# Optimization experiments

Measured on AMD Instinct MI355X. Metric: run time of the kernel, lower is better.

The kernel has to match this reference:

```python
import jax, jax.numpy as jnp
import numpy as np

B, N_KV, N_Q = 32, 4096, 8
D_INP, D_SLOT, HEADS, MLP_H = 256, 256, 4, 1024
ITERS = 3
EPS = 1e-8


def _ln(x, g, b, eps=1e-5):
    m = jnp.mean(x, axis=-1, keepdims=True)
    v = jnp.var(x, axis=-1, keepdims=True)
    return (x - m) * jax.lax.rsqrt(v + eps) * g + b


def setup_inputs() -> dict:
    key = jax.random.key(0)
    ks = jax.random.split(key, 12)
    def w(k, shape, fan_in):
        return jax.random.normal(k, shape, jnp.float32) / np.float32(np.sqrt(fan_in))
    return {
        "inputs": jax.random.normal(ks[0], (B, N_KV, D_INP), jnp.float32),
        "slots": jax.random.normal(ks[1], (B, N_Q, D_SLOT), jnp.float32),
        "ln_in_g": jnp.ones((D_INP,), jnp.float32), "ln_in_b": jnp.zeros((D_INP,), jnp.float32),
        "ln_slot_g": jnp.ones((D_SLOT,), jnp.float32), "ln_slot_b": jnp.zeros((D_SLOT,), jnp.float32),
        "ln_mlp_g": jnp.ones((D_SLOT,), jnp.float32), "ln_mlp_b": jnp.zeros((D_SLOT,), jnp.float32),
        "Wq": w(ks[2], (D_SLOT, D_SLOT), D_SLOT),
        "Wk": w(ks[3], (D_SLOT, D_INP), D_INP),
        "Wv": w(ks[4], (D_SLOT, D_INP), D_INP),
        "W_ih": w(ks[5], (3 * D_SLOT, D_SLOT), D_SLOT),
        "W_hh": w(ks[6], (3 * D_SLOT, D_SLOT), D_SLOT),
        "b_ih": jnp.zeros((3 * D_SLOT,), jnp.float32),
        "b_hh": jnp.zeros((3 * D_SLOT,), jnp.float32),
        "W1": w(ks[7], (MLP_H, D_SLOT), D_SLOT), "b1": jnp.zeros((MLP_H,), jnp.float32),
        "W2": w(ks[8], (D_SLOT, MLP_H), MLP_H), "b2": jnp.zeros((D_SLOT,), jnp.float32),
    }


def reference(inputs, slots, ln_in_g, ln_in_b, ln_slot_g, ln_slot_b, ln_mlp_g, ln_mlp_b,
              Wq, Wk, Wv, W_ih, W_hh, b_ih, b_hh, W1, b1, W2, b2):
    Bb, Nkv, _ = inputs.shape
    _, Nq, Ds = slots.shape
    hd = Ds // HEADS

    x = _ln(inputs, ln_in_g, ln_in_b)
    # k, v: [B, H, N_kv, hd]; k pre-scaled by hd**-0.5 as in the original
    k = (x @ Wk.T).reshape(Bb, Nkv, HEADS, hd).transpose(0, 2, 1, 3) * (hd ** -0.5)
    v = (x @ Wv.T).reshape(Bb, Nkv, HEADS, hd).transpose(0, 2, 1, 3)

    attn_vis = attn_temp = None
    for it in range(ITERS):
        if it == ITERS - 1:
            slots = jax.lax.stop_gradient(slots)
        slots_prev = slots
        s = _ln(slots, ln_slot_g, ln_slot_b)
        q = (s @ Wq.T).reshape(Bb, Nq, HEADS, hd).transpose(0, 2, 1, 3)  # [B,H,Nq,hd]
        logits = jnp.einsum('bhnd,bhqd->bhnq', k, q)  # [B,H,Nkv,Nq]
        # competing softmax: normalize jointly over (head, slot) per input token
        lt = logits.transpose(0, 2, 1, 3).reshape(Bb, Nkv, HEADS * Nq)
        attn = jax.nn.softmax(lt, axis=-1).reshape(Bb, Nkv, HEADS, Nq).transpose(0, 2, 1, 3)
        attn_vis = attn.sum(axis=1)   # [B, Nkv, Nq]
        attn_temp = attn_vis          # original recomputes the identical softmax; same values
        a = attn + EPS
        a = a / a.sum(axis=-2, keepdims=True)  # renormalize over N_kv
        updates = jnp.einsum('bhnq,bhnd->bhqd', a, v).transpose(0, 2, 1, 3).reshape(Bb, Nq, Ds)
        # GRU cell (torch GRUCell math)
        gx = updates @ W_ih.T + b_ih
        gh = slots_prev @ W_hh.T + b_hh
        xr, xz, xn = jnp.split(gx, 3, axis=-1)
        hr, hz, hn = jnp.split(gh, 3, axis=-1)
        r = jax.nn.sigmoid(xr + hr)
        z = jax.nn.sigmoid(xz + hz)
        n = jnp.tanh(xn + r * hn)
        slots = (1.0 - z) * n + z * slots_prev
        # MLP with residual
        m = _ln(slots, ln_mlp_g, ln_mlp_b)
        slots = slots + (jax.nn.relu(m @ W1.T + b1) @ W2.T + b2)
    return slots, attn_vis, attn_temp
```

## Files before the change

### kernel.cpp

```cpp
#include <hip/hip_runtime.h>
#include <math.h>


#define NKV   4096
#define DD    256
#define HQN   32
#define EPSR  1e-8f

#define WS_V      0
#define WS_A0     262144
#define WS_A1     263168
#define WS_C0     264192
#define WS_C1     265216
#define WS_SLOTA  266240
#define WS_SLOTB  331776
#define WS_WQT    397312
#define WS_QF     462848
#define WS_WPGXH  528384
#define WS_WFT    921600
#define WS_WHHT   1314816
#define WS_W1T    1413120
#define WS_W2T    1544192
#define WS_RS     1675264
#define WS_RM     1806336

typedef float f32x4 __attribute__((ext_vector_type(4)));
typedef short s16x8 __attribute__((ext_vector_type(8)));
typedef int   v2i   __attribute__((ext_vector_type(2)));

__device__ __forceinline__ unsigned bfr(float f) {
    unsigned u = __float_as_uint(f);
    return (u + 0x7fffu + ((u >> 16) & 1u)) >> 16;
}
__device__ __forceinline__ unsigned pk2(float lo, float hi) {
    return bfr(lo) | (bfr(hi) << 16);
}
__device__ __forceinline__ float bf2f(unsigned short us) {
    return __uint_as_float((unsigned)us << 16);
}
__device__ __forceinline__ float bflo(unsigned u) { return __uint_as_float(u << 16); }
__device__ __forceinline__ float bfhi(unsigned u) { return __uint_as_float(u & 0xffff0000u); }

__device__ __forceinline__ v2i tr_read(unsigned addr) {
    v2i d;
    asm volatile("ds_read_b64_tr_b16 %0, %1" : "=v"(d) : "v"(addr));
    return d;
}
__device__ __forceinline__ s16x8 mk_frag(v2i a, v2i b) {
    union { int i[4]; s16x8 s; } u;
    u.i[0] = a.x; u.i[1] = a.y; u.i[2] = b.x; u.i[3] = b.y;
    return u.s;
}

__global__ __launch_bounds__(256) void k_copy(const float* __restrict__ in,
                                              float* __restrict__ out, int n) {
    int i = blockIdx.x * 256 + threadIdx.x;
    if (i < n) out[i] = in[i];
}

__global__ __launch_bounds__(256) void k_tr(const float* __restrict__ in,
                                            float* __restrict__ out, int R, int C) {
    __shared__ float tile[32][33];
    int bx = blockIdx.x * 32, by = blockIdx.y * 32;
    int x = bx + threadIdx.x;
    for (int k = 0; k < 32; k += 8) {
        int y = by + threadIdx.y + k;
        if (x < C && y < R) tile[threadIdx.y + k][threadIdx.x] = in[(size_t)y * C + x];
    }
    __syncthreads();
    int r = by + threadIdx.x;
    for (int k = 0; k < 32; k += 8) {
        int c = bx + threadIdx.y + k;
        if (c < C && r < R) out[(size_t)c * R + r] = tile[threadIdx.x][threadIdx.y + k];
    }
}

__global__ __launch_bounds__(256) void k_wfold(
    const float* __restrict__ Wih, const float* __restrict__ Wv,
    unsigned* __restrict__ WfT2)
{
    __shared__ float wr[256];
    const int c = blockIdx.x, t = threadIdx.x;
    wr[t] = Wih[(size_t)c * 256 + t];
    __syncthreads();
    const float2* wv2 = (const float2*)Wv;
    #pragma unroll
    for (int pp = 0; pp < 2; ++pp) {
        int P = pp * 256 + t;
        int h = P >> 7, p = P & 127;
        float f0 = 0.f, f1 = 0.f;
        #pragma unroll 8
        for (int d = 0; d < 64; ++d) {
            float a = wr[h * 64 + d];
            float2 v = wv2[(size_t)(h * 64 + d) * 128 + p];
            f0 = fmaf(a, v.x, f0); f1 = fmaf(a, v.y, f1);
        }
        WfT2[(size_t)P * 768 + c] = pk2(f0, f1);
    }
}

__global__ __launch_bounds__(256) void k_trpack(
    const float* __restrict__ in, unsigned* __restrict__ out, int R, int C)
{
    const int c2 = blockIdx.x;
    const int t = threadIdx.x;
    for (int q = 0; q < R / 256; ++q) {
        int r = q * 256 + t;
        out[(size_t)c2 * R + r] = pk2(in[(size_t)r * C + 2 * c2],
                                      in[(size_t)r * C + 2 * c2 + 1]);
    }
}

__global__ __launch_bounds__(256) void k_prep_a(
    const float* __restrict__ slots, const float* __restrict__ g_s, const float* __restrict__ b_s,
    const float* __restrict__ wqt, float* __restrict__ qf_g,
    float* __restrict__ V_g, float* __restrict__ A0_g, float* __restrict__ A1_g)
{
    __shared__ float s_row[256];
    __shared__ float red[8];
    const int t = threadIdx.x;
    const int b = blockIdx.x, qi = blockIdx.y;
    const int lane = t & 63, w = t >> 6;

    #pragma unroll
    for (int h = 0; h < 4; ++h)
        V_g[((size_t)b * 32 + h * 8 + qi) * 256 + t] = 0.f;
    if (t < 4) { A0_g[b * 32 + t * 8 + qi] = 0.f; A1_g[b * 32 + t * 8 + qi] = 0.f; }

    float v = slots[((size_t)b * 8 + qi) * 256 + t];
    float s0 = v, s1 = v * v;
    #pragma unroll
    for (int o = 32; o >= 1; o >>= 1) { s0 += __shfl_xor(s0, o, 64); s1 += __shfl_xor(s1, o, 64); }
    if (lane == 0) { red[w] = s0; red[4 + w] = s1; }
    __syncthreads();
    {
        float m = (red[0] + red[1] + red[2] + red[3]) * (1.f / 256.f);
        float q2 = (red[4] + red[5] + red[6] + red[7]) * (1.f / 256.f);
        float rs = rsqrtf(q2 - m * m + 1e-5f);
        s_row[t] = (v - m) * rs * g_s[t] + b_s[t];
    }
    __syncthreads();

    float a = 0.f;
    #pragma unroll 8
    for (int j = 0; j < 256; ++j)
        a = fmaf(s_row[j], wqt[j * 256 + t], a);
    qf_g[((size_t)b * 8 + qi) * 256 + t] = a;
}

__global__ __launch_bounds__(256) void k_prep_b(
    const float* __restrict__ qf_g, const float* __restrict__ Wk,
    const float* __restrict__ g_in, const float* __restrict__ b_in,
    unsigned short* __restrict__ wp_bf, float* __restrict__ c0_g, float* __restrict__ c1_g)
{
    __shared__ float qs[512];
    __shared__ float redc[4096];
    const int t = threadIdx.x;
    const int b = blockIdx.x, h = blockIdx.y;
    const int lane = t & 63, w = t >> 6;
    const float LNS = 0.125f * 1.44269504f;

    #pragma unroll
    for (int rep = 0; rep < 2; ++rep) {
        int idx = rep * 256 + t;
        int qi = idx >> 6, d = idx & 63;
        qs[idx] = qf_g[((size_t)b * 8 + qi) * 256 + h * 64 + d];
    }
    __syncthreads();

    float a2[8];
    #pragma unroll
    for (int qi = 0; qi < 8; ++qi) a2[qi] = 0.f;
    #pragma unroll 4
    for (int d = 0; d < 64; ++d) {
        float wv = Wk[(size_t)(h * 64 + d) * 256 + t];
        #pragma unroll
        for (int qi = 0; qi < 8; ++qi) a2[qi] = fmaf(qs[qi * 64 + d], wv, a2[qi]);
    }
    const float gv = g_in[t], bv = b_in[t];
    #pragma unroll
    for (int qi = 0; qi < 8; ++qi) {
        float kv = LNS * a2[qi];
        float we = kv * gv;
        wp_bf[((size_t)b * HQN + h * 8 + qi) * 256 + t] = (unsigned short)bfr(we);
        redc[qi * 256 + t] = we;
        redc[2048 + qi * 256 + t] = kv * bv;
    }
    __syncthreads();
    #pragma unroll
    for (int rep = 0; rep < 2; ++rep) {
        int r = w * 2 + rep;
        float sv1 = redc[r * 256 + lane] + redc[r * 256 + 64 + lane] +
                    redc[r * 256 + 128 + lane] + redc[r * 256 + 192 + lane];
        float sv0 = redc[2048 + r * 256 + lane] + redc[2048 + r * 256 + 64 + lane] +
                    redc[2048 + r * 256 + 128 + lane] + redc[2048 + r * 256 + 192 + lane];
        #pragma unroll
        for (int o = 32; o >= 1; o >>= 1) {
            sv1 += __shfl_xor(sv1, o, 64);
            sv0 += __shfl_xor(sv0, o, 64);
        }
        if (lane == 0) {
            c1_g[b * 32 + h * 8 + r] = sv1;
            c0_g[b * 32 + h * 8 + r] = sv0;
        }
    }
}

template<int STATS, int WVIS>
__global__ __launch_bounds__(256, 4) void k_attn(
    const float* __restrict__ inp, const unsigned short* __restrict__ wp_bf,
    const float* __restrict__ c0_g, const float* __restrict__ c1_g,
    float* __restrict__ V_g, float* __restrict__ A0_g, float* __restrict__ A1_g,
    float* __restrict__ rs_g, float* __restrict__ rm_g,
    float* __restrict__ out_vis, float* __restrict__ out_temp)
{
    __shared__ unsigned short xb[16 * 520];
    __shared__ unsigned short wl[8192];
    __shared__ unsigned short pt[1024];
    __shared__ float stats[64];
    __shared__ float redm[64];
    __shared__ float reds[64];

    const int t = threadIdx.x;
    const int l = t & 63, w = t >> 6;
    const int g = l >> 4, li = l & 15;
    const int b = blockIdx.y, kb = blockIdx.x;

    char* xbB = (char*)xb;
    char* wlB = (char*)wl;
    char* ptB = (char*)pt;
    const int tok_s = t >> 3, seg8 = t & 7;

    {
        const uint4* wp4 = (const uint4*)wp_bf + ((size_t)b * 8192 + (t >> 3) * 256 + (t & 7) * 32) / 8;
        const int hq = t >> 3, sg = t & 7;
        #pragma unroll
        for (int q = 0; q < 4; ++q) {
            uint4 v = wp4[q];
            *(uint4*)(wlB + hq * 512 + (((sg * 4 + q) ^ (hq & 7)) * 16)) = v;
        }
    }

    const int Mt = w & 1, Nt = w >> 1;
    const int hqB = Nt * 16 + li;
    const float c0r = c0_g[b * 32 + hqB];
    const float c1r = c1_g[b * 32 + hqB];
    const int MtV = w >> 1, ntb = (w & 1) * 8;
    const int hqA = MtV * 16 + li;

    f32x4 av[8];
    #pragma unroll
    for (int u = 0; u < 8; ++u) av[u] = (f32x4){0.f, 0.f, 0.f, 0.f};
    float A0acc = 0.f, A1acc = 0.f;

    const unsigned xbase = (unsigned)(uintptr_t)xbB;
    const int cbase = kb * 4;

    #pragma unroll
    for (int ci = 0; ci < 4; ++ci) {
        const int n0 = (cbase + ci) * 32;

        const float4* row4 = (const float4*)(inp + ((size_t)b * NKV + n0 + tok_s) * 256);
        float4 ld[8];
        #pragma unroll
        for (int u = 0; u < 8; ++u) ld[u] = row4[(u >> 2) * 32 + seg8 * 4 + (u & 3)];

        if (!STATS) {
            if (t < 32) stats[t] = rs_g[b * 4096 + n0 + t];
            else if (t < 64) stats[t] = rm_g[b * 4096 + n0 + t - 32];
        }
        #pragma unroll
        for (int c = 0; c < 2; ++c) {
            int nt = seg8 + 8 * c;
            #pragma unroll
            for (int h = 0; h < 2; ++h) {
                float4 fa = ld[c * 4 + h * 2], fb = ld[c * 4 + h * 2 + 1];
                uint4 pk;
                pk.x = pk2(fa.x, fa.y); pk.y = pk2(fa.z, fa.w);
                pk.z = pk2(fb.x, fb.y); pk.w = pk2(fb.z, fb.w);
                *(uint4*)(xbB + nt * 1040 + tok_s * 32 + h * 16) = pk;
            }
        }
        if (STATS) {
            float s0 = 0.f, s1 = 0.f;
            #pragma unroll
            for (int u = 0; u < 8; ++u) {
                float4 v = ld[u];
                s0 += v.x + v.y + v.z + v.w;
                s1 = fmaf(v.x, v.x, s1); s1 = fmaf(v.y, v.y, s1);
                s1 = fmaf(v.z, v.z, s1); s1 = fmaf(v.w, v.w, s1);
            }
            s0 += __shfl_xor(s0, 1, 64); s1 += __shfl_xor(s1, 1, 64);
            s0 += __shfl_xor(s0, 2, 64); s1 += __shfl_xor(s1, 2, 64);
            s0 += __shfl_xor(s0, 4, 64); s1 += __shfl_xor(s1, 4, 64);
            float m  = s0 * (1.f / 256.f);
            float rs = rsqrtf(s1 * (1.f / 256.f) - m * m + 1e-5f);
            if (seg8 == 0) {
                stats[tok_s] = rs;
                stats[32 + tok_s] = rs * m;
                rs_g[b * 4096 + n0 + tok_s] = rs;
                rm_g[b * 4096 + n0 + tok_s] = rs * m;
            }
        }
        __syncthreads();

        f32x4 accS = (f32x4){0.f, 0.f, 0.f, 0.f};
        #pragma unroll
        for (int kk = 0; kk < 8; ++kk) {
            s16x8 af = *(const s16x8*)(xbB + (kk * 2 + (g >> 1)) * 1040 +
                                       (Mt * 16 + li) * 32 + (g & 1) * 16);
            s16x8 bf = *(const s16x8*)(wlB + hqB * 512 + (((kk * 4 + g) ^ (hqB & 7)) * 16));
            accS = __builtin_amdgcn_mfma_f32_16x16x32_bf16(af, bf, accS, 0, 0, 0);
        }

        float lg[4], rsv[4], rmv[4], mh[4], ex[4], aa[4];
        #pragma unroll
        for (int r = 0; r < 4; ++r) {
            int tokr = Mt * 16 + g * 4 + r;
            rsv[r] = stats[tokr];
            rmv[r] = stats[32 + tokr];
            lg[r] = fmaf(rsv[r], accS[r], fmaf(-rmv[r], c1r, c0r));
        }
        #pragma unroll
        for (int r = 0; r < 4; ++r) {
            float v = lg[r];
            v = fmaxf(v, __shfl_xor(v, 1, 64));
            v = fmaxf(v, __shfl_xor(v, 2, 64));
            v = fmaxf(v, __shfl_xor(v, 4, 64));
            v = fmaxf(v, __shfl_xor(v, 8, 64));
            mh[r] = v;
            ex[r] = exp2f(lg[r] - v);
            float s = ex[r];
            s += __shfl_xor(s, 1, 64);
            s += __shfl_xor(s, 2, 64);
            s += __shfl_xor(s, 4, 64);
            s += __shfl_xor(s, 8, 64);
            if (li == 0) {
                int tokr = Mt * 16 + g * 4 + r;
                redm[tokr * 2 + Nt] = v;
                reds[tokr * 2 + Nt] = s;
            }
        }
        __syncthreads();
        #pragma unroll
        for (int r = 0; r < 4; ++r) {
            int tokr = Mt * 16 + g * 4 + r;
            float m0 = redm[tokr * 2], m1 = redm[tokr * 2 + 1];
            float mx = fmaxf(m0, m1);
            float tot = reds[tokr * 2] * exp2f(m0 - mx) + reds[tokr * 2 + 1] * exp2f(m1 - mx);
            aa[r] = ex[r] * (exp2f(mh[r] - mx) / tot);
            A0acc += aa[r];
            A1acc = fmaf(aa[r], rmv[r], A1acc);
        }
        {
            uint2 pw;
            pw.x = pk2(aa[0] * rsv[0], aa[1] * rsv[1]);
            pw.y = pk2(aa[2] * rsv[2], aa[3] * rsv[3]);
            int tokb = Mt * 16 + g * 4;
            int slot = (tokb >> 3) ^ ((hqB >> 1) & 3);
            *(uint2*)(ptB + hqB * 64 + slot * 16 + (tokb & 7) * 2) = pw;
        }
        __syncthreads();

        if (WVIS) {
            int tk = t >> 3, q = t & 7;
            float sv = 0.f;
            #pragma unroll
            for (int h = 0; h < 4; ++h) {
                int hq = h * 8 + q;
                int slot = (tk >> 3) ^ ((hq >> 1) & 3);
                sv += bf2f(*(const unsigned short*)(ptB + hq * 64 + slot * 16 + (tk & 7) * 2));
            }
            float vv = sv / stats[tk];
            size_t o = ((size_t)b * NKV + n0 + tk) * 8 + q;
            out_vis[o] = vv; out_temp[o] = vv;
        }

        {
            s16x8 pa = *(const s16x8*)(ptB + hqA * 64 + ((g ^ ((hqA >> 1) & 3)) * 16));
            unsigned abase = xbase + g * 256 + li * 8;
            v2i t0a = tr_read(abase + (ntb + 0) * 1040);
            v2i t0b = tr_read(abase + (ntb + 0) * 1040 + 128);
            v2i t1a = tr_read(abase + (ntb + 1) * 1040);
            v2i t1b = tr_read(abase + (ntb + 1) * 1040 + 128);
            v2i t2a = tr_read(abase + (ntb + 2) * 1040);
            v2i t2b = tr_read(abase + (ntb + 2) * 1040 + 128);
            v2i t3a = tr_read(abase + (ntb + 3) * 1040);
            v2i t3b = tr_read(abase + (ntb + 3) * 1040 + 128);
            asm volatile("s_waitcnt lgkmcnt(0)" ::: "memory");
            __builtin_amdgcn_sched_barrier(0);
            av[0] = __builtin_amdgcn_mfma_f32_16x16x32_bf16(pa, mk_frag(t0a, t0b), av[0], 0, 0, 0);
            av[1] = __builtin_amdgcn_mfma_f32_16x16x32_bf16(pa, mk_frag(t1a, t1b), av[1], 0, 0, 0);
            av[2] = __builtin_amdgcn_mfma_f32_16x16x32_bf16(pa, mk_frag(t2a, t2b), av[2], 0, 0, 0);
            av[3] = __builtin_amdgcn_mfma_f32_16x16x32_bf16(pa, mk_frag(t3a, t3b), av[3], 0, 0, 0);
            v2i t4a = tr_read(abase + (ntb + 4) * 1040);
            v2i t4b = tr_read(abase + (ntb + 4) * 1040 + 128);
            v2i t5a = tr_read(abase + (ntb + 5) * 1040);
            v2i t5b = tr_read(abase + (ntb + 5) * 1040 + 128);
            v2i t6a = tr_read(abase + (ntb + 6) * 1040);
            v2i t6b = tr_read(abase + (ntb + 6) * 1040 + 128);
            v2i t7a = tr_read(abase + (ntb + 7) * 1040);
            v2i t7b = tr_read(abase + (ntb + 7) * 1040 + 128);
            asm volatile("s_waitcnt lgkmcnt(0)" ::: "memory");
            __builtin_amdgcn_sched_barrier(0);
            av[4] = __builtin_amdgcn_mfma_f32_16x16x32_bf16(pa, mk_frag(t4a, t4b), av[4], 0, 0, 0);
            av[5] = __builtin_amdgcn_mfma_f32_16x16x32_bf16(pa, mk_frag(t5a, t5b), av[5], 0, 0, 0);
            av[6] = __builtin_amdgcn_mfma_f32_16x16x32_bf16(pa, mk_frag(t6a, t6b), av[6], 0, 0, 0);
            av[7] = __builtin_amdgcn_mfma_f32_16x16x32_bf16(pa, mk_frag(t7a, t7b), av[7], 0, 0, 0);
        }
        __syncthreads();
    }

    A0acc += __shfl_xor(A0acc, 16, 64); A0acc += __shfl_xor(A0acc, 32, 64);
    A1acc += __shfl_xor(A1acc, 16, 64); A1acc += __shfl_xor(A1acc, 32, 64);
    if (g == 0) {
        atomicAdd(A0_g + b * 32 + hqB, A0acc);
        atomicAdd(A1_g + b * 32 + hqB, A1acc);
    }
    #pragma unroll
    for (int i = 0; i < 8; ++i) {
        int j = (ntb + i) * 16 + li;
        #pragma unroll
        for (int r = 0; r < 4; ++r) {
            int hq = MtV * 16 + g * 4 + r;
            atomicAdd(V_g + ((size_t)b * 32 + hq) * 256 + j, av[i][r]);
        }
    }
}

__global__ __launch_bounds__(256) void k_gates(
    const float* __restrict__ V_g, const float* __restrict__ A0_g,
    const float* __restrict__ A1_g,
    const float* __restrict__ g_in, const float* __restrict__ b_in,
    const float* __restrict__ slot_cur,
    const unsigned* __restrict__ WfT2, const unsigned* __restrict__ WhhT2,
    float* __restrict__ gxh, float* __restrict__ slot_nxt)
{
    __shared__ __align__(16) float aT[1024 * 4];
    const int t = threadIdx.x;
    const int rg = blockIdx.y;
    const int chunk = blockIdx.x;
    const int row0 = rg * 4;
    float acc0 = 0.f, acc1 = 0.f, acc2 = 0.f, acc3 = 0.f;

    if (chunk == 0) {
        #pragma unroll
        for (int rr = 0; rr < 4; ++rr)
            slot_nxt[(size_t)(row0 + rr) * 256 + t] = 0.f;
    }

    if (chunk < 3) {
        const int b = rg >> 1, qi0 = (rg & 1) * 4;
        const float gt = g_in[t], bt = b_in[t];
        #pragma unroll
        for (int kk = 0; kk < 4; ++kk) {
            float4 y4;
            #pragma unroll
            for (int rr = 0; rr < 4; ++rr) {
                int hq = kk * 8 + qi0 + rr;
                float A0 = A0_g[b * 32 + hq], A1 = A1_g[b * 32 + hq];
                float den = A0 + EPSR * (float)NKV;
                float vv = V_g[((size_t)b * 32 + hq) * 256 + t];
                float yv = (gt * (vv - A1) + bt * A0) / den;
                ((float*)&y4)[rr] = yv;
            }
            *(float4*)(aT + (kk * 256 + t) * 4) = y4;
        }
        __syncthreads();
        const unsigned* wp = WfT2 + chunk * 256 + t;
        #pragma unroll 4
        for (int k2 = 0; k2 < 512; ++k2) {
            unsigned wv = wp[(size_t)k2 * 768];
            float w0 = bflo(wv), w1 = bfhi(wv);
            float4 a0 = *(const float4*)(aT + 8 * k2);
            float4 a1 = *(const float4*)(aT + 8 * k2 + 4);
            acc0 = fmaf(a0.x, w0, acc0); acc0 = fmaf(a1.x, w1, acc0);
            acc1 = fmaf(a0.y, w0, acc1); acc1 = fmaf(a1.y, w1, acc1);
            acc2 = fmaf(a0.z, w0, acc2); acc2 = fmaf(a1.z, w1, acc2);
            acc3 = fmaf(a0.w, w0, acc3); acc3 = fmaf(a1.w, w1, acc3);
        }
        float* go = gxh + (size_t)row0 * 1536 + chunk * 256 + t;
        go[0] = acc0; go[1536] = acc1; go[3072] = acc2; go[4608] = acc3;
    } else {
        const int gc = chunk - 3;
        {
            float4 y4;
            #pragma unroll
            for (int rr = 0; rr < 4; ++rr)
                ((float*)&y4)[rr] = slot_cur[(size_t)(row0 + rr) * 256 + t];
            *(float4*)(aT + t * 4) = y4;
        }
        __syncthreads();
        const unsigned* wp = WhhT2 + gc * 256 + t;
        #pragma unroll 4
        for (int k2 = 0; k2 < 128; ++k2) {
            unsigned wv = wp[(size_t)k2 * 768];
            float w0 = bflo(wv), w1 = bfhi(wv);
            float4 a0 = *(const float4*)(aT + 8 * k2);
            float4 a1 = *(const float4*)(aT + 8 * k2 + 4);
            acc0 = fmaf(a0.x, w0, acc0); acc0 = fmaf(a1.x, w1, acc0);
            acc1 = fmaf(a0.y, w0, acc1); acc1 = fmaf(a1.y, w1, acc1);
            acc2 = fmaf(a0.z, w0, acc2); acc2 = fmaf(a1.z, w1, acc2);
            acc3 = fmaf(a0.w, w0, acc3); acc3 = fmaf(a1.w, w1, acc3);
        }
        float* go = gxh + (size_t)row0 * 1536 + 768 + gc * 256 + t;
        go[0] = acc0; go[1536] = acc1; go[3072] = acc2; go[4608] = acc3;
    }
}

__global__ __launch_bounds__(256) void k_mlp(
    const float* __restrict__ gxh, const float* __restrict__ slot_cur,
    const float* __restrict__ bih, const float* __restrict__ bhh,
    const float* __restrict__ gm, const float* __restrict__ bm,
    const unsigned* __restrict__ W1T2, const float* __restrict__ b1,
    const unsigned* __restrict__ W2T2, const float* __restrict__ b2,
    float* __restrict__ slot_nxt)
{
    __shared__ __align__(16) float mT[1024];
    __shared__ float sm_l[4][256];
    __shared__ float h1_l[4][256];
    __shared__ float lnst[8];
    const int t = threadIdx.x;
    const int rg = blockIdx.y, chunk = blockIdx.x;
    const int row0 = rg * 4;
    const int lane = t & 63, w = t >> 6;

    const float bi0 = bih[t], bi1 = bih[256 + t], bi2 = bih[512 + t];
    const float bh0 = bhh[t], bh1 = bhh[256 + t], bh2 = bhh[512 + t];
    float smid[4];
    #pragma unroll
    for (int rr = 0; rr < 4; ++rr) {
        const float* gr = gxh + (size_t)(row0 + rr) * 1536;
        float gx0 = gr[t], gx1 = gr[256 + t], gx2 = gr[512 + t];
        float gh0 = gr[768 + t], gh1 = gr[1024 + t], gh2 = gr[1280 + t];
        float spv = slot_cur[(size_t)(row0 + rr) * 256 + t];
        float r = 1.f / (1.f + __expf(-(gx0 + bi0 + gh0 + bh0)));
        float z = 1.f / (1.f + __expf(-(gx1 + bi1 + gh1 + bh1)));
        float n = tanhf(gx2 + bi2 + r * (gh2 + bh2));
        smid[rr] = (1.f - z) * n + z * spv;
        sm_l[rr][t] = smid[rr];
    }
    __syncthreads();
    {
        float4 v = *(const float4*)(&sm_l[w][lane * 4]);
        float s0 = v.x + v.y + v.z + v.w;
        float s1 = v.x * v.x + v.y * v.y + v.z * v.z + v.w * v.w;
        #pragma unroll
        for (int o = 32; o >= 1; o >>= 1) { s0 += __shfl_xor(s0, o, 64); s1 += __shfl_xor(s1, o, 64); }
        if (lane == 0) {
            float mu = s0 * (1.f / 256.f);
            lnst[w * 2] = mu;
            lnst[w * 2 + 1] = rsqrtf(s1 * (1.f / 256.f) - mu * mu + 1e-5f);
        }
    }
    __syncthreads();
    {
        const float gmt = gm[t], bmt = bm[t];
        float4 m4;
        #pragma unroll
        for (int rr = 0; rr < 4; ++rr)
            ((float*)&m4)[rr] = (smid[rr] - lnst[rr * 2]) * lnst[rr * 2 + 1] * gmt + bmt;
        *(float4*)(mT + t * 4) = m4;
    }
    __syncthreads();

    {
        float acc0 = 0.f, acc1 = 0.f, acc2 = 0.f, acc3 = 0.f;
        const unsigned* wp = W1T2 + chunk * 256 + t;
        #pragma unroll 4
        for (int k2 = 0; k2 < 128; ++k2) {
            unsigned wv = wp[(size_t)k2 * 1024];
            float w0 = bflo(wv), w1 = bfhi(wv);
            float4 a0 = *(const float4*)(mT + 8 * k2);
            float4 a1 = *(const float4*)(mT + 8 * k2 + 4);
            acc0 = fmaf(a0.x, w0, acc0); acc0 = fmaf(a1.x, w1, acc0);
            acc1 = fmaf(a0.y, w0, acc1); acc1 = fmaf(a1.y, w1, acc1);
            acc2 = fmaf(a0.z, w0, acc2); acc2 = fmaf(a1.z, w1, acc2);
            acc3 = fmaf(a0.w, w0, acc3); acc3 = fmaf(a1.w, w1, acc3);
        }
        const float b1t = b1[chunk * 256 + t];
        h1_l[0][t] = fmaxf(acc0 + b1t, 0.f);
        h1_l[1][t] = fmaxf(acc1 + b1t, 0.f);
        h1_l[2][t] = fmaxf(acc2 + b1t, 0.f);
        h1_l[3][t] = fmaxf(acc3 + b1t, 0.f);
    }
    __syncthreads();

    {
        float o0 = 0.f, o1 = 0.f, o2 = 0.f, o3 = 0.f;
        const unsigned* wp = W2T2 + (size_t)(chunk * 128) * 256 + t;
        #pragma unroll 4
        for (int k2 = 0; k2 < 128; ++k2) {
            unsigned wv = wp[(size_t)k2 * 256];
            float w0 = bflo(wv), w1 = bfhi(wv);
            float a00 = h1_l[0][2 * k2], a01 = h1_l[0][2 * k2 + 1];
            float a10 = h1_l[1][2 * k2], a11 = h1_l[1][2 * k2 + 1];
            float a20 = h1_l[2][2 * k2], a21 = h1_l[2][2 * k2 + 1];
            float a30 = h1_l[3][2 * k2], a31 = h1_l[3][2 * k2 + 1];
            o0 = fmaf(a00, w0, o0); o0 = fmaf(a01, w1, o0);
            o1 = fmaf(a10, w0, o1); o1 = fmaf(a11, w1, o1);
            o2 = fmaf(a20, w0, o2); o2 = fmaf(a21, w1, o2);
            o3 = fmaf(a30, w0, o3); o3 = fmaf(a31, w1, o3);
        }
        const float b2t = b2[t];
        float base0 = (chunk == 0) ? smid[0] + b2t : 0.f;
        float base1 = (chunk == 0) ? smid[1] + b2t : 0.f;
        float base2 = (chunk == 0) ? smid[2] + b2t : 0.f;
        float base3 = (chunk == 0) ? smid[3] + b2t : 0.f;
        atomicAdd(slot_nxt + (size_t)(row0 + 0) * 256 + t, o0 + base0);
        atomicAdd(slot_nxt + (size_t)(row0 + 1) * 256 + t, o1 + base1);
        atomicAdd(slot_nxt + (size_t)(row0 + 2) * 256 + t, o2 + base2);
        atomicAdd(slot_nxt + (size_t)(row0 + 3) * 256 + t, o3 + base3);
    }
}

extern "C" void kernel_launch(void* const* d_in, const int* in_sizes, int n_in,
                              void* d_out, int out_size, void* d_ws, size_t ws_size,
                              hipStream_t stream) {
    const float* inp     = (const float*)d_in[0];
    const float* slots0  = (const float*)d_in[1];
    const float* ln_in_g = (const float*)d_in[2];
    const float* ln_in_b = (const float*)d_in[3];
    const float* ln_s_g  = (const float*)d_in[4];
    const float* ln_s_b  = (const float*)d_in[5];
    const float* ln_m_g  = (const float*)d_in[6];
    const float* ln_m_b  = (const float*)d_in[7];
    const float* Wq  = (const float*)d_in[8];
    const float* Wk  = (const float*)d_in[9];
    const float* Wv  = (const float*)d_in[10];
    const float* Wih = (const float*)d_in[11];
    const float* Whh = (const float*)d_in[12];
    const float* bih = (const float*)d_in[13];
    const float* bhh = (const float*)d_in[14];
    const float* W1  = (const float*)d_in[15];
    const float* b1  = (const float*)d_in[16];
    const float* W2  = (const float*)d_in[17];
    const float* b2  = (const float*)d_in[18];

    float* ws = (float*)d_ws;
    float* V_g   = ws + WS_V;
    float* A0_g  = ws + WS_A0;
    float* A1_g  = ws + WS_A1;
    float* c0_g  = ws + WS_C0;
    float* c1_g  = ws + WS_C1;
    float* slotA = ws + WS_SLOTA;
    float* slotB = ws + WS_SLOTB;
    float* wqt   = ws + WS_WQT;
    float* qf_g  = ws + WS_QF;
    float* gxh   = ws + WS_WPGXH;
    unsigned short* wp_bf = (unsigned short*)(ws + WS_WPGXH);
    unsigned* WfT2  = (unsigned*)(ws + WS_WFT);
    unsigned* WhhT2 = (unsigned*)(ws + WS_WHHT);
    unsigned* W1T2  = (unsigned*)(ws + WS_W1T);
    unsigned* W2T2  = (unsigned*)(ws + WS_W2T);
    float* rs_g = ws + WS_RS;
    float* rm_g = ws + WS_RM;

    float* out_slots = (float*)d_out;
    float* out_vis   = out_slots + 32 * 8 * 256;
    float* out_temp  = out_vis + 32 * 4096 * 8;

    k_tr<<<dim3(8, 8), dim3(32, 8), 0, stream>>>(Wq, wqt, 256, 256);
    k_wfold<<<768, 256, 0, stream>>>(Wih, Wv, WfT2);
    k_trpack<<<128, 256, 0, stream>>>(Whh, WhhT2, 768, 256);
    k_trpack<<<128, 256, 0, stream>>>(W1, W1T2, 1024, 256);
    k_trpack<<<512, 256, 0, stream>>>(W2, W2T2, 256, 1024);
    k_copy<<<256, 256, 0, stream>>>(slots0, slotA, 65536);

    for (int it = 0; it < 3; ++it) {
        float* cur = (it & 1) ? slotB : slotA;
        float* nxt = (it & 1) ? slotA : slotB;
        k_prep_a<<<dim3(32, 8), 256, 0, stream>>>(cur, ln_s_g, ln_s_b, wqt, qf_g,
                                                  V_g, A0_g, A1_g);
        k_prep_b<<<dim3(32, 4), 256, 0, stream>>>(qf_g, Wk, ln_in_g, ln_in_b,
                                                  wp_bf, c0_g, c1_g);
        if (it == 0)
            k_attn<1, 0><<<dim3(32, 32), 256, 0, stream>>>(
                inp, wp_bf, c0_g, c1_g, V_g, A0_g, A1_g, rs_g, rm_g, out_vis, out_temp);
        else if (it == 1)
            k_attn<0, 0><<<dim3(32, 32), 256, 0, stream>>>(
                inp, wp_bf, c0_g, c1_g, V_g, A0_g, A1_g, rs_g, rm_g, out_vis, out_temp);
        else
            k_attn<0, 1><<<dim3(32, 32), 256, 0, stream>>>(
                inp, wp_bf, c0_g, c1_g, V_g, A0_g, A1_g, rs_g, rm_g, out_vis, out_temp);
        k_gates<<<dim3(6, 64), 256, 0, stream>>>(
            V_g, A0_g, A1_g, ln_in_g, ln_in_b, cur, WfT2, WhhT2, gxh, nxt);
        k_mlp<<<dim3(4, 64), 256, 0, stream>>>(
            gxh, cur, bih, bhh, ln_m_g, ln_m_b, W1T2, b1, W2T2, b2, nxt);
    }
    k_copy<<<256, 256, 0, stream>>>(slotB, out_slots, 65536);
}
```

Measured before the change: 495.3 us.

## Double-buffer input tiles in attention and replace V atomics with partial-sum reduction

The attention kernel now double-buffers the bf16 input tile and LN stats in shared memory. The next chunk's global load is issued before the current chunk's MFMA work, so load latency overlaps compute. The per-block float atomicAdds into V are replaced by plain stores to a per-block partial buffer, which a new k_vred kernel then sums, removing atomic contention. The trade-offs are doubled shared memory for the x tile, a dropped occupancy hint in launch_bounds, an extra kernel launch per iteration, and additional partial-buffer global traffic.

```diff
diff --git a/kernel.cpp b/kernel.cpp
--- a/kernel.cpp
+++ b/kernel.cpp
@@ -23,6 +23,7 @@
 #define WS_W2T    1544192
 #define WS_RS     1675264
 #define WS_RM     1806336
+#define WS_VPART  1937408
 
 typedef float f32x4 __attribute__((ext_vector_type(4)));
 typedef short s16x8 __attribute__((ext_vector_type(8)));
@@ -114,7 +115,7 @@
 __global__ __launch_bounds__(256) void k_prep_a(
     const float* __restrict__ slots, const float* __restrict__ g_s, const float* __restrict__ b_s,
     const float* __restrict__ wqt, float* __restrict__ qf_g,
-    float* __restrict__ V_g, float* __restrict__ A0_g, float* __restrict__ A1_g)
+    float* __restrict__ A0_g, float* __restrict__ A1_g)
 {
     __shared__ float s_row[256];
     __shared__ float red[8];
@@ -122,9 +123,6 @@
     const int b = blockIdx.x, qi = blockIdx.y;
     const int lane = t & 63, w = t >> 6;
 
-    #pragma unroll
-    for (int h = 0; h < 4; ++h)
-        V_g[((size_t)b * 32 + h * 8 + qi) * 256 + t] = 0.f;
     if (t < 4) { A0_g[b * 32 + t * 8 + qi] = 0.f; A1_g[b * 32 + t * 8 + qi] = 0.f; }
 
     float v = slots[((size_t)b * 8 + qi) * 256 + t];
@@ -206,18 +204,64 @@
     }
 }
 
+__device__ __forceinline__ void load_x(const float* __restrict__ inp, int b, int n0,
+                                       int tok_s, int seg8, float4* ld) {
+    const float4* row4 = (const float4*)(inp + ((size_t)b * NKV + n0 + tok_s) * 256);
+    #pragma unroll
+    for (int u = 0; u < 8; ++u) ld[u] = row4[(u >> 2) * 32 + seg8 * 4 + (u & 3)];
+}
+
+__device__ __forceinline__ void pack_x(const float4* ld, char* dst, int tok_s, int seg8) {
+    #pragma unroll
+    for (int c = 0; c < 2; ++c) {
+        int nt = seg8 + 8 * c;
+        #pragma unroll
+        for (int h = 0; h < 2; ++h) {
+            float4 fa = ld[c * 4 + h * 2], fb = ld[c * 4 + h * 2 + 1];
+            uint4 pk;
+            pk.x = pk2(fa.x, fa.y); pk.y = pk2(fa.z, fa.w);
+            pk.z = pk2(fb.x, fb.y); pk.w = pk2(fb.z, fb.w);
+            *(uint4*)(dst + nt * 1040 + tok_s * 32 + h * 16) = pk;
+        }
+    }
+}
+
+__device__ __forceinline__ void calc_stats(const float4* ld, float* sb,
+                                           float* __restrict__ rs_g, float* __restrict__ rm_g,
+                                           int b, int n0, int tok_s, int seg8) {
+    float s0 = 0.f, s1 = 0.f;
+    #pragma unroll
+    for (int u = 0; u < 8; ++u) {
+        float4 v = ld[u];
+        s0 += v.x + v.y + v.z + v.w;
+        s1 = fmaf(v.x, v.x, s1); s1 = fmaf(v.y, v.y, s1);
+        s1 = fmaf(v.z, v.z, s1); s1 = fmaf(v.w, v.w, s1);
+    }
+    s0 += __shfl_xor(s0, 1, 64); s1 += __shfl_xor(s1, 1, 64);
+    s0 += __shfl_xor(s0, 2, 64); s1 += __shfl_xor(s1, 2, 64);
+    s0 += __shfl_xor(s0, 4, 64); s1 += __shfl_xor(s1, 4, 64);
+    float m  = s0 * (1.f / 256.f);
+    float rs = rsqrtf(s1 * (1.f / 256.f) - m * m + 1e-5f);
+    if (seg8 == 0) {
+        sb[tok_s] = rs;
+        sb[32 + tok_s] = rs * m;
+        rs_g[b * 4096 + n0 + tok_s] = rs;
+        rm_g[b * 4096 + n0 + tok_s] = rs * m;
+    }
+}
+
 template<int STATS, int WVIS>
-__global__ __launch_bounds__(256, 4) void k_attn(
+__global__ __launch_bounds__(256) void k_attn(
     const float* __restrict__ inp, const unsigned short* __restrict__ wp_bf,
     const float* __restrict__ c0_g, const float* __restrict__ c1_g,
-    float* __restrict__ V_g, float* __restrict__ A0_g, float* __restrict__ A1_g,
+    float* __restrict__ vpart, float* __restrict__ A0_g, float* __restrict__ A1_g,
     float* __restrict__ rs_g, float* __restrict__ rm_g,
     float* __restrict__ out_vis, float* __restrict__ out_temp)
 {
-    __shared__ unsigned short xb[16 * 520];
+    __shared__ unsigned short xb[2][8320];
     __shared__ unsigned short wl[8192];
     __shared__ unsigned short pt[1024];
-    __shared__ float stats[64];
+    __shared__ float stats[2][64];
     __shared__ float redm[64];
     __shared__ float reds[64];
 
@@ -230,6 +274,7 @@
     char* wlB = (char*)wl;
     char* ptB = (char*)pt;
     const int tok_s = t >> 3, seg8 = t & 7;
+    const int cbase = kb * 4;
 
     {
         const uint4* wp4 = (const uint4*)wp_bf + ((size_t)b * 8192 + (t >> 3) * 256 + (t & 7) * 32) / 8;
@@ -254,60 +299,35 @@
     float A0acc = 0.f, A1acc = 0.f;
 
     const unsigned xbase = (unsigned)(uintptr_t)xbB;
-    const int cbase = kb * 4;
+
+    {
+        float4 ldA[8];
+        load_x(inp, b, cbase * 32, tok_s, seg8, ldA);
+        if (STATS) {
+            calc_stats(ldA, &stats[0][0], rs_g, rm_g, b, cbase * 32, tok_s, seg8);
+        } else {
+            if (t < 32) stats[0][t] = rs_g[b * 4096 + cbase * 32 + t];
+            else if (t < 64) stats[0][t] = rm_g[b * 4096 + cbase * 32 + t - 32];
+        }
+        pack_x(ldA, xbB, tok_s, seg8);
+    }
+    __syncthreads();
 
     #pragma unroll
     for (int ci = 0; ci < 4; ++ci) {
+        const int cur = ci & 1, nxt = cur ^ 1;
         const int n0 = (cbase + ci) * 32;
-
-        const float4* row4 = (const float4*)(inp + ((size_t)b * NKV + n0 + tok_s) * 256);
-        float4 ld[8];
-        #pragma unroll
-        for (int u = 0; u < 8; ++u) ld[u] = row4[(u >> 2) * 32 + seg8 * 4 + (u & 3)];
-
-        if (!STATS) {
-            if (t < 32) stats[t] = rs_g[b * 4096 + n0 + t];
-            else if (t < 64) stats[t] = rm_g[b * 4096 + n0 + t - 32];
-        }
-        #pragma unroll
-        for (int c = 0; c < 2; ++c) {
-            int nt = seg8 + 8 * c;
-            #pragma unroll
-            for (int h = 0; h < 2; ++h) {
-                float4 fa = ld[c * 4 + h * 2], fb = ld[c * 4 + h * 2 + 1];
-                uint4 pk;
-                pk.x = pk2(fa.x, fa.y); pk.y = pk2(fa.z, fa.w);
-                pk.z = pk2(fb.x, fb.y); pk.w = pk2(fb.z, fb.w);
-                *(uint4*)(xbB + nt * 1040 + tok_s * 32 + h * 16) = pk;
-            }
-        }
-        if (STATS) {
-            float s0 = 0.f, s1 = 0.f;
-            #pragma unroll
-            for (int u = 0; u < 8; ++u) {
-                float4 v = ld[u];
-                s0 += v.x + v.y + v.z + v.w;
-                s1 = fmaf(v.x, v.x, s1); s1 = fmaf(v.y, v.y, s1);
-                s1 = fmaf(v.z, v.z, s1); s1 = fmaf(v.w, v.w, s1);
-            }
-            s0 += __shfl_xor(s0, 1, 64); s1 += __shfl_xor(s1, 1, 64);
-            s0 += __shfl_xor(s0, 2, 64); s1 += __shfl_xor(s1, 2, 64);
-            s0 += __shfl_xor(s0, 4, 64); s1 += __shfl_xor(s1, 4, 64);
-            float m  = s0 * (1.f / 256.f);
-            float rs = rsqrtf(s1 * (1.f / 256.f) - m * m + 1e-5f);
-            if (seg8 == 0) {
-                stats[tok_s] = rs;
-                stats[32 + tok_s] = rs * m;
-                rs_g[b * 4096 + n0 + tok_s] = rs;
-                rm_g[b * 4096 + n0 + tok_s] = rs * m;
-            }
-        }
-        __syncthreads();
+        char* xc = xbB + cur * 16640;
+        char* xn = xbB + nxt * 16640;
+
+        float4 ldN[8];
+        if (ci < 3) load_x(inp, b, n0 + 32, tok_s, seg8, ldN);
+        __builtin_amdgcn_sched_barrier(0);
 
         f32x4 accS = (f32x4){0.f, 0.f, 0.f, 0.f};
         #pragma unroll
         for (int kk = 0; kk < 8; ++kk) {
-            s16x8 af = *(const s16x8*)(xbB + (kk * 2 + (g >> 1)) * 1040 +
+            s16x8 af = *(const s16x8*)(xc + (kk * 2 + (g >> 1)) * 1040 +
                                        (Mt * 16 + li) * 32 + (g & 1) * 16);
             s16x8 bf = *(const s16x8*)(wlB + hqB * 512 + (((kk * 4 + g) ^ (hqB & 7)) * 16));
             accS = __builtin_amdgcn_mfma_f32_16x16x32_bf16(af, bf, accS, 0, 0, 0);
@@ -317,8 +337,8 @@
         #pragma unroll
         for (int r = 0; r < 4; ++r) {
             int tokr = Mt * 16 + g * 4 + r;
-            rsv[r] = stats[tokr];
-            rmv[r] = stats[32 + tokr];
+            rsv[r] = stats[cur][tokr];
+            rmv[r] = stats[cur][32 + tokr];
             lg[r] = fmaf(rsv[r], accS[r], fmaf(-rmv[r], c1r, c0r));
         }
         #pragma unroll
@@ -371,14 +391,24 @@
                 int slot = (tk >> 3) ^ ((hq >> 1) & 3);
                 sv += bf2f(*(const unsigned short*)(ptB + hq * 64 + slot * 16 + (tk & 7) * 2));
             }
-            float vv = sv / stats[tk];
+            float vv = sv / stats[cur][tk];
             size_t o = ((size_t)b * NKV + n0 + tk) * 8 + q;
             out_vis[o] = vv; out_temp[o] = vv;
         }
 
+        if (ci < 3) {
+            if (STATS) {
+                calc_stats(ldN, &stats[nxt][0], rs_g, rm_g, b, n0 + 32, tok_s, seg8);
+            } else {
+                if (t < 32) stats[nxt][t] = rs_g[b * 4096 + n0 + 32 + t];
+                else if (t < 64) stats[nxt][t] = rm_g[b * 4096 + n0 + 32 + t - 32];
+            }
+            pack_x(ldN, xn, tok_s, seg8);
+        }
+
         {
             s16x8 pa = *(const s16x8*)(ptB + hqA * 64 + ((g ^ ((hqA >> 1) & 3)) * 16));
-            unsigned abase = xbase + g * 256 + li * 8;
+            unsigned abase = xbase + cur * 16640 + g * 256 + li * 8;
             v2i t0a = tr_read(abase + (ntb + 0) * 1040);
             v2i t0b = tr_read(abase + (ntb + 0) * 1040 + 128);
             v2i t1a = tr_read(abase + (ntb + 1) * 1040);
@@ -417,15 +447,29 @@
         atomicAdd(A0_g + b * 32 + hqB, A0acc);
         atomicAdd(A1_g + b * 32 + hqB, A1acc);
     }
+    float* vp = vpart + ((size_t)(b * 32 + kb) * 32) * 256;
     #pragma unroll
     for (int i = 0; i < 8; ++i) {
         int j = (ntb + i) * 16 + li;
         #pragma unroll
         for (int r = 0; r < 4; ++r) {
             int hq = MtV * 16 + g * 4 + r;
-            atomicAdd(V_g + ((size_t)b * 32 + hq) * 256 + j, av[i][r]);
-        }
-    }
+            vp[(size_t)hq * 256 + j] = av[i][r];
+        }
+    }
+}
+
+__global__ __launch_bounds__(256) void k_vred(
+    const float* __restrict__ vpart, float* __restrict__ V_g)
+{
+    const int t = threadIdx.x;
+    const int b = blockIdx.x, hq = blockIdx.y;
+    const float* p = vpart + ((size_t)(b * 32) * 32 + hq) * 256 + t;
+    float s = 0.f;
+    #pragma unroll 8
+    for (int kb = 0; kb < 32; ++kb)
+        s += p[(size_t)kb * 8192];
+    V_g[((size_t)b * 32 + hq) * 256 + t] = s;
 }
 
 __global__ __launch_bounds__(256) void k_gates(
@@ -653,8 +697,9 @@
     unsigned* WhhT2 = (unsigned*)(ws + WS_WHHT);
     unsigned* W1T2  = (unsigned*)(ws + WS_W1T);
     unsigned* W2T2  = (unsigned*)(ws + WS_W2T);
-    float* rs_g = ws + WS_RS;
-    float* rm_g = ws + WS_RM;
+    float* rs_g  = ws + WS_RS;
+    float* rm_g  = ws + WS_RM;
+    float* vpart = ws + WS_VPART;
 
     float* out_slots = (float*)d_out;
     float* out_vis   = out_slots + 32 * 8 * 256;
@@ -671,18 +716,19 @@
         float* cur = (it & 1) ? slotB : slotA;
         float* nxt = (it & 1) ? slotA : slotB;
         k_prep_a<<<dim3(32, 8), 256, 0, stream>>>(cur, ln_s_g, ln_s_b, wqt, qf_g,
-                                                  V_g, A0_g, A1_g);
+                                                  A0_g, A1_g);
         k_prep_b<<<dim3(32, 4), 256, 0, stream>>>(qf_g, Wk, ln_in_g, ln_in_b,
                                                   wp_bf, c0_g, c1_g);
         if (it == 0)
             k_attn<1, 0><<<dim3(32, 32), 256, 0, stream>>>(
-                inp, wp_bf, c0_g, c1_g, V_g, A0_g, A1_g, rs_g, rm_g, out_vis, out_temp);
+                inp, wp_bf, c0_g, c1_g, vpart, A0_g, A1_g, rs_g, rm_g, out_vis, out_temp);
         else if (it == 1)
             k_attn<0, 0><<<dim3(32, 32), 256, 0, stream>>>(
-                inp, wp_bf, c0_g, c1_g, V_g, A0_g, A1_g, rs_g, rm_g, out_vis, out_temp);
+                inp, wp_bf, c0_g, c1_g, vpart, A0_g, A1_g, rs_g, rm_g, out_vis, out_temp);
         else
             k_attn<0, 1><<<dim3(32, 32), 256, 0, stream>>>(
-                inp, wp_bf, c0_g, c1_g, V_g, A0_g, A1_g, rs_g, rm_g, out_vis, out_temp);
+                inp, wp_bf, c0_g, c1_g, vpart, A0_g, A1_g, rs_g, rm_g, out_vis, out_temp);
+        k_vred<<<dim3(32, 32), 256, 0, stream>>>(vpart, V_g);
         k_gates<<<dim3(6, 64), 256, 0, stream>>>(
             V_g, A0_g, A1_g, ln_in_g, ln_in_b, cur, WfT2, WhhT2, gxh, nxt);
         k_mlp<<<dim3(4, 64), 256, 0, stream>>>(
```

After: 476.3 us. 3.8% less time.
